# Performance work log

Measured on AMD Instinct MI355X. Metric: run time of the kernel, lower is better.

Reference implementation:

```python
import jax, jax.numpy as jnp
import numpy as np

D_THRESH = 0.5  # init arg `dist`


def setup_inputs() -> dict:
    key = jax.random.key(0)
    k1, k2 = jax.random.split(key)
    N, M, C = 20000, 25000, 3
    pointcloud = jax.random.uniform(k1, (N, C), dtype=jnp.float32)
    pointcloud_padding = jax.random.uniform(k2, (M, C), dtype=jnp.float32)
    return {"pointcloud": pointcloud, "pointcloud_padding": pointcloud_padding}


def reference(pointcloud, pointcloud_padding):
    # torch.cdist(padding, pointcloud): Euclidean distance matrix [M, N]
    # via the GEMM formulation ||a||^2 + ||b||^2 - 2 a.b (matches torch's path)
    a2 = jnp.sum(pointcloud_padding * pointcloud_padding, axis=1)[:, None]  # [M,1]
    b2 = jnp.sum(pointcloud * pointcloud, axis=1)[None, :]                  # [1,N]
    ab = pointcloud_padding @ pointcloud.T                                  # [M,N]
    dist = jnp.sqrt(jnp.maximum(a2 + b2 - 2.0 * ab, 0.0))                   # [M,N]
    # count neighbors within radius, per pointcloud point
    counts = jnp.sum(dist <= D_THRESH, axis=0).astype(jnp.int32)            # [N]
    out = counts.reshape(-1, 1)[: pointcloud.shape[0]]                      # [N,1]
    return out
```

## Files before the change

### kernel.cpp

```cpp
#include <hip/hip_runtime.h>

typedef short  bf16x8 __attribute__((ext_vector_type(8)));

#define JS      13
#define STREAMS (JS * 4)
#define TI      128
#define DEPTH   2

__device__ __forceinline__ unsigned short f2bf(float x) {
    unsigned u = __builtin_bit_cast(unsigned, x);
    u += 0x7FFF + ((u >> 16) & 1);
    return (unsigned short)(u >> 16);
}
__device__ __forceinline__ float bf2f(unsigned short h) {
    unsigned u = ((unsigned)h) << 16;
    return __builtin_bit_cast(float, u);
}

__global__ __launch_bounds__(256) void dens_pack_kernel(
    const float* __restrict__ pad, uint4* __restrict__ ws,
    int* __restrict__ out, int M, int mtot, int N)
{
    const int j = blockIdx.x * 256 + threadIdx.x;
    if (j < N) out[j] = 0;
    if (j >= mtot) return;

    float qx = 0.f, qy = 0.f, qz = 0.f;
    float negc = -1.0e6f;
    if (j < M) {
        qx = pad[3 * j]; qy = pad[3 * j + 1]; qz = pad[3 * j + 2];
        negc = 0.125f - 0.5f * (qx * qx + qy * qy + qz * qz);
    }
    const unsigned short xh = f2bf(qx), yh = f2bf(qy), zh = f2bf(qz);
    const unsigned short xl = f2bf(qx - bf2f(xh));
    const unsigned short yl = f2bf(qy - bf2f(yh));
    const unsigned short zl = f2bf(qz - bf2f(zh));
    const unsigned short ch = f2bf(negc);
    const unsigned short cl = f2bf(negc - bf2f(ch));

    uint4 p0, p1;
    p0.x = (unsigned)xh | ((unsigned)yh << 16);
    p0.y = (unsigned)zh | ((unsigned)xl << 16);
    p0.z = (unsigned)yl | ((unsigned)zl << 16);
    p0.w = (unsigned)xh | ((unsigned)yh << 16);
    p1.x = (unsigned)zh | ((unsigned)xl << 16);
    p1.y = (unsigned)yl | ((unsigned)zl << 16);
    p1.z = (unsigned)ch | ((unsigned)cl << 16);
    p1.w = 0x3F803F80u;
    ws[j]        = p0;
    ws[mtot + j] = p1;
}

__device__ __forceinline__ void make_bfrag(const float* __restrict__ pc,
                                           int i, int N, int half, bf16x8& B)
{
    float px = 0.f, py = 0.f, pz = 0.f;
    float ha = 3.0e38f;
    if (i < N) {
        px = pc[3 * i]; py = pc[3 * i + 1]; pz = pc[3 * i + 2];
        ha = 0.5f * (px * px + py * py + pz * pz);
    }
    const float nha = -ha;
    const unsigned short nhh = f2bf(nha);
    const unsigned short nhl = f2bf(nha - bf2f(nhh));
    const short xh = (short)f2bf(px), yh = (short)f2bf(py), zh = (short)f2bf(pz);
    const short xl = (short)f2bf(px - bf2f((unsigned short)xh));
    const short yl = (short)f2bf(py - bf2f((unsigned short)yh));
    const short zl = (short)f2bf(pz - bf2f((unsigned short)zh));
    const short ONE = (short)0x3F80;
    const bf16x8 Blo = {xh, yh, zh, xh, yh, zh, xl, yl};
    const bf16x8 Bhi = {zl, xl, yl, zl, ONE, ONE, (short)nhh, (short)nhl};
    B = half ? Bhi : Blo;
}

#define CONS(R0,R1,R2,R3,R4,R5,R6,R7,R8,R9,RA,RB,RC,RD,RE,RF, CA, CB) \
    "v_ashrrev_i32 " R0 ", 31, " R0 "\n\t" \
    "v_ashrrev_i32 " R1 ", 31, " R1 "\n\t" \
    "v_ashrrev_i32 " R2 ", 31, " R2 "\n\t" \
    "v_ashrrev_i32 " R3 ", 31, " R3 "\n\t" \
    "v_ashrrev_i32 " R4 ", 31, " R4 "\n\t" \
    "v_ashrrev_i32 " R5 ", 31, " R5 "\n\t" \
    "v_ashrrev_i32 " R6 ", 31, " R6 "\n\t" \
    "v_ashrrev_i32 " R7 ", 31, " R7 "\n\t" \
    "v_ashrrev_i32 " R8 ", 31, " R8 "\n\t" \
    "v_ashrrev_i32 " R9 ", 31, " R9 "\n\t" \
    "v_ashrrev_i32 " RA ", 31, " RA "\n\t" \
    "v_ashrrev_i32 " RB ", 31, " RB "\n\t" \
    "v_ashrrev_i32 " RC ", 31, " RC "\n\t" \
    "v_ashrrev_i32 " RD ", 31, " RD "\n\t" \
    "v_ashrrev_i32 " RE ", 31, " RE "\n\t" \
    "v_ashrrev_i32 " RF ", 31, " RF "\n\t" \
    "v_add3_u32 " CA ", " R0 ", " R1 ", " CA "\n\t" \
    "v_add3_u32 " CB ", " R2 ", " R3 ", " CB "\n\t" \
    "v_add3_u32 " CA ", " R4 ", " R5 ", " CA "\n\t" \
    "v_add3_u32 " CB ", " R6 ", " R7 ", " CB "\n\t" \
    "v_add3_u32 " CA ", " R8 ", " R9 ", " CA "\n\t" \
    "v_add3_u32 " CB ", " RA ", " RB ", " CB "\n\t" \
    "v_add3_u32 " CA ", " RC ", " RD ", " CA "\n\t" \
    "v_add3_u32 " CB ", " RE ", " RF ", " CB "\n\t"

#define CONS_D0(CA, CB) \
    CONS("v32","v33","v34","v35","v36","v37","v38","v39", \
         "v40","v41","v42","v43","v44","v45","v46","v47", CA, CB)
#define CONS_D1(CA, CB) \
    CONS("v48","v49","v50","v51","v52","v53","v54","v55", \
         "v56","v57","v58","v59","v60","v61","v62","v63", CA, CB)

#define VISIT(AR) \
    "s_waitcnt vmcnt(1)\n\t" \
    "v_mfma_f32_32x32x16_bf16 v[32:47], " AR ", %9,  v[64:79]\n\t" \
    "v_mfma_f32_32x32x16_bf16 v[48:63], " AR ", %10, v[64:79]\n\t" \
    "s_nop 7\n\t" \
    "s_nop 2\n\t" \
    CONS_D0("%0", "%1") \
    "v_mfma_f32_32x32x16_bf16 v[32:47], " AR ", %11, v[64:79]\n\t" \
    CONS_D1("%2", "%3") \
    "v_mfma_f32_32x32x16_bf16 v[48:63], " AR ", %12, v[64:79]\n\t" \
    "global_load_dwordx4 " AR ", v[88:89], off\n\t" \
    "v_add_co_u32 v88, vcc, 0x6800, v88\n\t" \
    "v_addc_co_u32 v89, vcc, 0, v89, vcc\n\t" \
    CONS_D0("%4", "%5") \
    CONS_D1("%6", "%7")

__global__ __launch_bounds__(256, 4) void dens_mfma_kernel(
    const float* __restrict__ pc,
    const char*  __restrict__ wsA,
    int* __restrict__ out,
    int N, int iters, int p1off, int visits)
{
    const int lane = threadIdx.x & 63;
    const int w    = threadIdx.x >> 6;
    const int n    = lane & 31;
    const int half = lane >> 5;

    const int ibase = blockIdx.x * TI;
    bf16x8 B0, B1, B2, B3;
    make_bfrag(pc, ibase + n,      N, half, B0);
    make_bfrag(pc, ibase + 32 + n, N, half, B1);
    make_bfrag(pc, ibase + 64 + n, N, half, B2);
    make_bfrag(pc, ibase + 96 + n, N, half, B3);

    const int stream = blockIdx.y * 4 + w;
    const unsigned long long ax =
        (unsigned long long)(wsA + (half ? p1off : 0) + n * 16 + (size_t)stream * 512);
    const unsigned xlo = (unsigned)ax, xhi = (unsigned)(ax >> 32);

    int it = iters;
    int c0a = 0, c0b = 0, c1a = 0, c1b = 0, c2a = 0, c2b = 0, c3a = 0, c3b = 0;

    asm volatile(
        "v_mov_b32 v88, %13\n\t"
        "v_mov_b32 v89, %14\n\t"
        "v_mov_b32 v64, 0\n\t" "v_mov_b32 v65, 0\n\t"
        "v_mov_b32 v66, 0\n\t" "v_mov_b32 v67, 0\n\t"
        "v_mov_b32 v68, 0\n\t" "v_mov_b32 v69, 0\n\t"
        "v_mov_b32 v70, 0\n\t" "v_mov_b32 v71, 0\n\t"
        "v_mov_b32 v72, 0\n\t" "v_mov_b32 v73, 0\n\t"
        "v_mov_b32 v74, 0\n\t" "v_mov_b32 v75, 0\n\t"
        "v_mov_b32 v76, 0\n\t" "v_mov_b32 v77, 0\n\t"
        "v_mov_b32 v78, 0\n\t" "v_mov_b32 v79, 0\n\t"
        "global_load_dwordx4 v[80:83], v[88:89], off\n\t"
        "v_add_co_u32 v88, vcc, 0x6800, v88\n\t"
        "v_addc_co_u32 v89, vcc, 0, v89, vcc\n\t"
        "global_load_dwordx4 v[84:87], v[88:89], off\n\t"
        "v_add_co_u32 v88, vcc, 0x6800, v88\n\t"
        "v_addc_co_u32 v89, vcc, 0, v89, vcc\n\t"
        "Ldens%=:\n\t"
        VISIT("v[80:83]")
        VISIT("v[84:87]")
        "s_sub_u32 %8, %8, 1\n\t"
        "s_cmp_lg_u32 %8, 0\n\t"
        "s_cbranch_scc1 Ldens%=\n\t"
        : "+v"(c0a), "+v"(c0b), "+v"(c1a), "+v"(c1b),
          "+v"(c2a), "+v"(c2b), "+v"(c3a), "+v"(c3b), "+s"(it)
        : "v"(B0), "v"(B1), "v"(B2), "v"(B3), "v"(xlo), "v"(xhi)
        : "vcc", "scc", "memory",
          "v32","v33","v34","v35","v36","v37","v38","v39",
          "v40","v41","v42","v43","v44","v45","v46","v47",
          "v48","v49","v50","v51","v52","v53","v54","v55",
          "v56","v57","v58","v59","v60","v61","v62","v63",
          "v64","v65","v66","v67","v68","v69","v70","v71",
          "v72","v73","v74","v75","v76","v77","v78","v79",
          "v80","v81","v82","v83","v84","v85","v86","v87",
          "v88","v89");

    const int base = 32 * visits;
    int t0 = c0a + c0b;  t0 += __shfl_xor(t0, 32);
    int t1 = c1a + c1b;  t1 += __shfl_xor(t1, 32);
    int t2 = c2a + c2b;  t2 += __shfl_xor(t2, 32);
    int t3 = c3a + c3b;  t3 += __shfl_xor(t3, 32);

    __shared__ int red[4][TI];
    if (lane < 32) {
        red[w][n]      = base + t0;
        red[w][n + 32] = base + t1;
        red[w][n + 64] = base + t2;
        red[w][n + 96] = base + t3;
    }
    __syncthreads();
    if (threadIdx.x < TI) {
        const int ii = ibase + threadIdx.x;
        if (ii < N) {
            const int s = red[0][threadIdx.x] + red[1][threadIdx.x] +
                          red[2][threadIdx.x] + red[3][threadIdx.x];
            atomicAdd(&out[ii], s);
        }
    }
}

extern "C" void kernel_launch(void* const* d_in, const int* in_sizes, int n_in,
                              void* d_out, int out_size, void* d_ws, size_t ws_size,
                              hipStream_t stream) {
    const float* pc  = (const float*)d_in[0];
    const float* pad = (const float*)d_in[1];
    int* out = (int*)d_out;

    const int N = in_sizes[0] / 3;
    const int M = in_sizes[1] / 3;
    const int jt = (M + 31) / 32;
    int visits = (jt + STREAMS - 1) / STREAMS;
    if (visits & 1) visits++;
    const int jtp  = (visits + DEPTH) * STREAMS;
    const int mtot = jtp * 32;

    dens_pack_kernel<<<(mtot + 255) / 256, 256, 0, stream>>>(
        pad, (uint4*)d_ws, out, M, mtot, N);

    dim3 grid((N + TI - 1) / TI, JS);
    dens_mfma_kernel<<<grid, 256, 0, stream>>>(
        pc, (const char*)d_ws, out, N, visits / 2, mtot * 16, visits);
}
```

Measured before the change: 85.57 us.

## Stage padding tiles through LDS per block instead of per-wave global streams

```diff
diff --git a/kernel.cpp b/kernel.cpp
--- a/kernel.cpp
+++ b/kernel.cpp
@@ -2,10 +2,10 @@
 
 typedef short  bf16x8 __attribute__((ext_vector_type(8)));
 
-#define JS      13
-#define STREAMS (JS * 4)
-#define TI      128
-#define DEPTH   2
+#define CHUNK_TILES 32
+#define CHUNKS      25
+#define TOTTILES    (CHUNK_TILES * CHUNKS)
+#define MROWS       (TOTTILES * 32)
 
 __device__ __forceinline__ unsigned short f2bf(float x) {
     unsigned u = __builtin_bit_cast(unsigned, x);
@@ -18,12 +18,10 @@
 }
 
 __global__ __launch_bounds__(256) void dens_pack_kernel(
-    const float* __restrict__ pad, uint4* __restrict__ ws,
-    int* __restrict__ out, int M, int mtot, int N)
+    const float* __restrict__ pad, uint4* __restrict__ ws, int M)
 {
     const int j = blockIdx.x * 256 + threadIdx.x;
-    if (j < N) out[j] = 0;
-    if (j >= mtot) return;
+    if (j >= MROWS) return;
 
     float qx = 0.f, qy = 0.f, qz = 0.f;
     float negc = -1.0e6f;
@@ -47,8 +45,9 @@
     p1.y = (unsigned)yl | ((unsigned)zl << 16);
     p1.z = (unsigned)ch | ((unsigned)cl << 16);
     p1.w = 0x3F803F80u;
-    ws[j]        = p0;
-    ws[mtot + j] = p1;
+    const int T = j >> 5, n = j & 31;
+    ws[T * 64 + n]      = p0;
+    ws[T * 64 + 32 + n] = p1;
 }
 
 __device__ __forceinline__ void make_bfrag(const float* __restrict__ pc,
@@ -106,104 +105,91 @@
     CONS("v48","v49","v50","v51","v52","v53","v54","v55", \
          "v56","v57","v58","v59","v60","v61","v62","v63", CA, CB)
 
-#define VISIT(AR) \
-    "s_waitcnt vmcnt(1)\n\t" \
-    "v_mfma_f32_32x32x16_bf16 v[32:47], " AR ", %9,  v[64:79]\n\t" \
-    "v_mfma_f32_32x32x16_bf16 v[48:63], " AR ", %10, v[64:79]\n\t" \
-    "s_nop 7\n\t" \
-    "s_nop 2\n\t" \
-    CONS_D0("%0", "%1") \
-    "v_mfma_f32_32x32x16_bf16 v[32:47], " AR ", %11, v[64:79]\n\t" \
-    CONS_D1("%2", "%3") \
-    "v_mfma_f32_32x32x16_bf16 v[48:63], " AR ", %12, v[64:79]\n\t" \
-    "global_load_dwordx4 " AR ", v[88:89], off\n\t" \
-    "v_add_co_u32 v88, vcc, 0x6800, v88\n\t" \
-    "v_addc_co_u32 v89, vcc, 0, v89, vcc\n\t" \
-    CONS_D0("%4", "%5") \
-    CONS_D1("%6", "%7")
-
-__global__ __launch_bounds__(256, 4) void dens_mfma_kernel(
+__global__ __launch_bounds__(512, 4) void dens_mfma_kernel(
     const float* __restrict__ pc,
-    const char*  __restrict__ wsA,
-    int* __restrict__ out,
-    int N, int iters, int p1off, int visits)
+    const uint4* __restrict__ wsA,
+    int* __restrict__ out, int N)
 {
-    const int lane = threadIdx.x & 63;
-    const int w    = threadIdx.x >> 6;
+    __shared__ uint4 stage[2048];
+    __shared__ int   red[8][32];
+
+    const int tid  = threadIdx.x;
+    const int lane = tid & 63;
+    const int w    = tid >> 6;
     const int n    = lane & 31;
     const int half = lane >> 5;
 
-    const int ibase = blockIdx.x * TI;
-    bf16x8 B0, B1, B2, B3;
-    make_bfrag(pc, ibase + n,      N, half, B0);
-    make_bfrag(pc, ibase + 32 + n, N, half, B1);
-    make_bfrag(pc, ibase + 64 + n, N, half, B2);
-    make_bfrag(pc, ibase + 96 + n, N, half, B3);
-
-    const int stream = blockIdx.y * 4 + w;
-    const unsigned long long ax =
-        (unsigned long long)(wsA + (half ? p1off : 0) + n * 16 + (size_t)stream * 512);
-    const unsigned xlo = (unsigned)ax, xhi = (unsigned)(ax >> 32);
-
-    int it = iters;
-    int c0a = 0, c0b = 0, c1a = 0, c1b = 0, c2a = 0, c2b = 0, c3a = 0, c3b = 0;
-
-    asm volatile(
-        "v_mov_b32 v88, %13\n\t"
-        "v_mov_b32 v89, %14\n\t"
-        "v_mov_b32 v64, 0\n\t" "v_mov_b32 v65, 0\n\t"
-        "v_mov_b32 v66, 0\n\t" "v_mov_b32 v67, 0\n\t"
-        "v_mov_b32 v68, 0\n\t" "v_mov_b32 v69, 0\n\t"
-        "v_mov_b32 v70, 0\n\t" "v_mov_b32 v71, 0\n\t"
-        "v_mov_b32 v72, 0\n\t" "v_mov_b32 v73, 0\n\t"
-        "v_mov_b32 v74, 0\n\t" "v_mov_b32 v75, 0\n\t"
-        "v_mov_b32 v76, 0\n\t" "v_mov_b32 v77, 0\n\t"
-        "v_mov_b32 v78, 0\n\t" "v_mov_b32 v79, 0\n\t"
-        "global_load_dwordx4 v[80:83], v[88:89], off\n\t"
-        "v_add_co_u32 v88, vcc, 0x6800, v88\n\t"
-        "v_addc_co_u32 v89, vcc, 0, v89, vcc\n\t"
-        "global_load_dwordx4 v[84:87], v[88:89], off\n\t"
-        "v_add_co_u32 v88, vcc, 0x6800, v88\n\t"
-        "v_addc_co_u32 v89, vcc, 0, v89, vcc\n\t"
-        "Ldens%=:\n\t"
-        VISIT("v[80:83]")
-        VISIT("v[84:87]")
-        "s_sub_u32 %8, %8, 1\n\t"
-        "s_cmp_lg_u32 %8, 0\n\t"
-        "s_cbranch_scc1 Ldens%=\n\t"
-        : "+v"(c0a), "+v"(c0b), "+v"(c1a), "+v"(c1b),
-          "+v"(c2a), "+v"(c2b), "+v"(c3a), "+v"(c3b), "+s"(it)
-        : "v"(B0), "v"(B1), "v"(B2), "v"(B3), "v"(xlo), "v"(xhi)
-        : "vcc", "scc", "memory",
-          "v32","v33","v34","v35","v36","v37","v38","v39",
-          "v40","v41","v42","v43","v44","v45","v46","v47",
-          "v48","v49","v50","v51","v52","v53","v54","v55",
-          "v56","v57","v58","v59","v60","v61","v62","v63",
-          "v64","v65","v66","v67","v68","v69","v70","v71",
-          "v72","v73","v74","v75","v76","v77","v78","v79",
-          "v80","v81","v82","v83","v84","v85","v86","v87",
-          "v88","v89");
-
-    const int base = 32 * visits;
-    int t0 = c0a + c0b;  t0 += __shfl_xor(t0, 32);
-    int t1 = c1a + c1b;  t1 += __shfl_xor(t1, 32);
-    int t2 = c2a + c2b;  t2 += __shfl_xor(t2, 32);
-    int t3 = c3a + c3b;  t3 += __shfl_xor(t3, 32);
-
-    __shared__ int red[4][TI];
-    if (lane < 32) {
-        red[w][n]      = base + t0;
-        red[w][n + 32] = base + t1;
-        red[w][n + 64] = base + t2;
-        red[w][n + 96] = base + t3;
-    }
+    bf16x8 B;
+    make_bfrag(pc, blockIdx.x * 32 + n, N, half, B);
+
+    const unsigned lds_base =
+        (unsigned)(unsigned long long)(&stage[0]) + (unsigned)(w * 1024 + half * 512 + n * 16);
+
+    uint4 r0 = wsA[tid],       r1 = wsA[512 + tid];
+    uint4 r2 = wsA[1024 + tid], r3 = wsA[1536 + tid];
+
+    int cA = 0, cB = 0;
+
+    for (int c = 0; c < CHUNKS; ++c) {
+        stage[tid] = r0; stage[512 + tid] = r1;
+        stage[1024 + tid] = r2; stage[1536 + tid] = r3;
+        __syncthreads();
+        if (c + 1 < CHUNKS) {
+            const int b = (c + 1) * 2048 + tid;
+            r0 = wsA[b]; r1 = wsA[b + 512]; r2 = wsA[b + 1024]; r3 = wsA[b + 1536];
+        }
+        asm volatile(
+            "v_mov_b32 v64, 0\n\t" "v_mov_b32 v65, 0\n\t"
+            "v_mov_b32 v66, 0\n\t" "v_mov_b32 v67, 0\n\t"
+            "v_mov_b32 v68, 0\n\t" "v_mov_b32 v69, 0\n\t"
+            "v_mov_b32 v70, 0\n\t" "v_mov_b32 v71, 0\n\t"
+            "v_mov_b32 v72, 0\n\t" "v_mov_b32 v73, 0\n\t"
+            "v_mov_b32 v74, 0\n\t" "v_mov_b32 v75, 0\n\t"
+            "v_mov_b32 v76, 0\n\t" "v_mov_b32 v77, 0\n\t"
+            "v_mov_b32 v78, 0\n\t" "v_mov_b32 v79, 0\n\t"
+            "ds_read_b128 v[80:83], %3\n\t"
+            "ds_read_b128 v[84:87], %3 offset:8192\n\t"
+            "ds_read_b128 v[88:91], %3 offset:16384\n\t"
+            "ds_read_b128 v[92:95], %3 offset:24576\n\t"
+            "s_waitcnt lgkmcnt(2)\n\t"
+            "v_mfma_f32_32x32x16_bf16 v[32:47], v[80:83], %2, v[64:79]\n\t"
+            "v_mfma_f32_32x32x16_bf16 v[48:63], v[84:87], %2, v[64:79]\n\t"
+            "s_nop 7\n\t"
+            "s_nop 2\n\t"
+            CONS_D0("%0", "%1")
+            "s_waitcnt lgkmcnt(0)\n\t"
+            "v_mfma_f32_32x32x16_bf16 v[32:47], v[88:91], %2, v[64:79]\n\t"
+            CONS_D1("%0", "%1")
+            "v_mfma_f32_32x32x16_bf16 v[48:63], v[92:95], %2, v[64:79]\n\t"
+            "s_nop 7\n\t"
+            "s_nop 2\n\t"
+            CONS_D0("%0", "%1")
+            CONS_D1("%0", "%1")
+            : "+v"(cA), "+v"(cB)
+            : "v"(B), "v"(lds_base)
+            : "memory",
+              "v32","v33","v34","v35","v36","v37","v38","v39",
+              "v40","v41","v42","v43","v44","v45","v46","v47",
+              "v48","v49","v50","v51","v52","v53","v54","v55",
+              "v56","v57","v58","v59","v60","v61","v62","v63",
+              "v64","v65","v66","v67","v68","v69","v70","v71",
+              "v72","v73","v74","v75","v76","v77","v78","v79",
+              "v80","v81","v82","v83","v84","v85","v86","v87",
+              "v88","v89","v90","v91","v92","v93","v94","v95");
+        __syncthreads();
+    }
+
+    int t = 1600 + cA + cB;
+    t += __shfl_xor(t, 32);
+    if (lane < 32) red[w][n] = t;
     __syncthreads();
-    if (threadIdx.x < TI) {
-        const int ii = ibase + threadIdx.x;
+    if (tid < 32) {
+        const int ii = blockIdx.x * 32 + tid;
         if (ii < N) {
-            const int s = red[0][threadIdx.x] + red[1][threadIdx.x] +
-                          red[2][threadIdx.x] + red[3][threadIdx.x];
-            atomicAdd(&out[ii], s);
+            int s = 0;
+            #pragma unroll
+            for (int k = 0; k < 8; ++k) s += red[k][tid];
+            out[ii] = s;
         }
     }
 }
@@ -217,16 +203,10 @@
 
     const int N = in_sizes[0] / 3;
     const int M = in_sizes[1] / 3;
-    const int jt = (M + 31) / 32;
-    int visits = (jt + STREAMS - 1) / STREAMS;
-    if (visits & 1) visits++;
-    const int jtp  = (visits + DEPTH) * STREAMS;
-    const int mtot = jtp * 32;
-
-    dens_pack_kernel<<<(mtot + 255) / 256, 256, 0, stream>>>(
-        pad, (uint4*)d_ws, out, M, mtot, N);
-
-    dim3 grid((N + TI - 1) / TI, JS);
-    dens_mfma_kernel<<<grid, 256, 0, stream>>>(
-        pc, (const char*)d_ws, out, N, visits / 2, mtot * 16, visits);
-}
+
+    dens_pack_kernel<<<(MROWS + 255) / 256, 256, 0, stream>>>(
+        pad, (uint4*)d_ws, M);
+
+    dens_mfma_kernel<<<(N + 31) / 32, 512, 0, stream>>>(
+        pc, (const uint4*)d_ws, out, N);
+}
```

Measured after the change: 100.5 us. 17.4% more time.
